# Kernel tuning notes

Hardware: AMD Instinct MI355X
Metric: run time of the kernel (lower is better)

The kernel has to match this reference:

```python
import jax, jax.numpy as jnp
import numpy as np

B, N, D_IN, D, K, H, ITERS = 128, 4096, 64, 64, 8, 128, 3
SCALE = D ** -0.5
EPS_ATTN = 1e-8
EPS_LN = 1e-5


def layer_norm(x, g, b):
    m = jnp.mean(x, axis=-1, keepdims=True)
    v = jnp.mean((x - m) ** 2, axis=-1, keepdims=True)
    return (x - m) * jax.lax.rsqrt(v + EPS_LN) * g + b


def setup_inputs() -> dict:
    key = jax.random.key(0)
    ks = jax.random.split(key, 16)
    s = 0.05
    return {
        "inputs": jax.random.normal(ks[0], (B, N, D_IN), dtype=jnp.float32),
        "noise": jax.random.normal(ks[1], (B, K, D), dtype=jnp.float32),
        "slots_mu": jax.random.normal(ks[2], (1, 1, D), dtype=jnp.float32),
        "slots_sigma": jax.random.normal(ks[3], (1, 1, D), dtype=jnp.float32),
        "Wq": jax.random.normal(ks[4], (D, D), dtype=jnp.float32) * s,
        "Wk": jax.random.normal(ks[5], (D_IN, D), dtype=jnp.float32) * s,
        "Wv": jax.random.normal(ks[6], (D_IN, D), dtype=jnp.float32) * s,
        "W_ih": jax.random.normal(ks[7], (3 * D, D), dtype=jnp.float32) * s,
        "W_hh": jax.random.normal(ks[8], (3 * D, D), dtype=jnp.float32) * s,
        "b_ih": jnp.zeros((3 * D,), dtype=jnp.float32),
        "b_hh": jnp.zeros((3 * D,), dtype=jnp.float32),
        "mlp_W1": jax.random.normal(ks[9], (D, H), dtype=jnp.float32) * s,
        "mlp_b1": jnp.zeros((H,), dtype=jnp.float32),
        "mlp_W2": jax.random.normal(ks[10], (H, D), dtype=jnp.float32) * s,
        "mlp_b2": jnp.zeros((D,), dtype=jnp.float32),
        "ln_in_g": jnp.ones((D_IN,), dtype=jnp.float32),
        "ln_in_b": jnp.zeros((D_IN,), dtype=jnp.float32),
        "ln_s_g": jnp.ones((D,), dtype=jnp.float32),
        "ln_s_b": jnp.zeros((D,), dtype=jnp.float32),
        "ln_ff_g": jnp.ones((D,), dtype=jnp.float32),
        "ln_ff_b": jnp.zeros((D,), dtype=jnp.float32),
    }


def reference(inputs, noise, slots_mu, slots_sigma, Wq, Wk, Wv,
              W_ih, W_hh, b_ih, b_hh, mlp_W1, mlp_b1, mlp_W2, mlp_b2,
              ln_in_g, ln_in_b, ln_s_g, ln_s_b, ln_ff_g, ln_ff_b):
    # slots = Normal(mu, sigma) with externally supplied standard noise
    slots = slots_mu + slots_sigma * noise                      # [B,K,D]
    x = layer_norm(inputs, ln_in_g, ln_in_b)                     # [B,N,D_IN]
    k = x @ Wk                                                   # [B,N,D]
    v = x @ Wv                                                   # [B,N,D]

    for _ in range(ITERS):
        slots_prev = slots
        s = layer_norm(slots, ln_s_g, ln_s_b)
        q = s @ Wq                                               # [B,K,D]
        dots = jnp.einsum('bid,bjd->bij', q, k) * SCALE          # [B,K,N]
        attn = jax.nn.softmax(dots, axis=1) + EPS_ATTN           # softmax over slots
        attn_n = attn / jnp.sum(attn, axis=-1, keepdims=True)
        updates = jnp.einsum('bjd,bij->bid', v, attn_n)          # [B,K,D]

        # single-step GRU (torch nn.GRU gate order: reset, update, new)
        gx = updates @ W_ih.T + b_ih                             # [B,K,3D]
        gh = slots_prev @ W_hh.T + b_hh                          # [B,K,3D]
        gx_r, gx_z, gx_n = jnp.split(gx, 3, axis=-1)
        gh_r, gh_z, gh_n = jnp.split(gh, 3, axis=-1)
        r = jax.nn.sigmoid(gx_r + gh_r)
        z = jax.nn.sigmoid(gx_z + gh_z)
        n = jnp.tanh(gx_n + r * gh_n)
        slots = (1.0 - z) * n + z * slots_prev

        slots = layer_norm(slots, ln_ff_g, ln_ff_b)
        slots = slots + (jax.nn.relu(slots @ mlp_W1 + mlp_b1) @ mlp_W2 + mlp_b2)
    return slots
```

## Files before the change

kernel.cpp:

```cpp
#include <hip/hip_runtime.h>
#include <hip/hip_bf16.h>

typedef unsigned int u32;
typedef unsigned short u16;
typedef __attribute__((ext_vector_type(8))) short short8;
typedef __attribute__((ext_vector_type(4))) float f32x4;
typedef __attribute__((ext_vector_type(2))) u32 u32x2;

#define B_      128
#define N_      4096
#define K_      8
#define SCALE_  0.125f
#define EPS_A   1e-8f
#define EPS_LN  1e-5f

__device__ __forceinline__ float bf_lo(u32 u){ union{u32 v; float f;} x; x.v = u<<16; return x.f; }
__device__ __forceinline__ u16 f2bf(float f){
  union{float f; u32 v;} x; x.f = f;
  u32 v = x.v;
  return (u16)((v + 0x7fffu + ((v>>16)&1u))>>16);
}
__device__ __forceinline__ float wsum64(float v){
  #pragma unroll
  for (int off=32; off; off>>=1) v += __shfl_xor(v, off, 64);
  return v;
}
__device__ __forceinline__ void gll16(const void* g, void* l){
  __builtin_amdgcn_global_load_lds(
      (const __attribute__((address_space(1))) void*)g,
      (__attribute__((address_space(3))) void*)l, 16, 0, 0);
}

__global__ void prep_t(const float* __restrict__ Wih, const float* __restrict__ Whh,
                       const float* __restrict__ Wq,  const float* __restrict__ Wk,
                       float* __restrict__ WihT, float* __restrict__ WhhT,
                       float* __restrict__ Wqk, int* __restrict__ flags){
  int t = threadIdx.x;
  if (blockIdx.x == 0 && t < B_) flags[t] = 0;
  if (blockIdx.x < 48){
    int idx = blockIdx.x*256 + t;
    int g = idx>>6, d = idx&63;
    WihT[d*192+g] = Wih[idx];
    WhhT[d*192+g] = Whh[idx];
  } else {
    __shared__ float WkL[64*65];
    int bi = blockIdx.x - 48;
    #pragma unroll
    for (int k=0;k<16;++k){
      int idx = t + k*256;
      int d = idx>>6, m = idx&63;
      WkL[m*65+d] = Wk[idx];
    }
    __syncthreads();
    int a = bi*4 + (t>>6), d = t&63;
    float acc = 0.f;
    #pragma unroll 8
    for (int m=0;m<64;++m) acc += Wq[a*64+m]*WkL[m*65+d];
    Wqk[a*64+d] = acc;
  }
}

__device__ __forceinline__ void tile_attn(
    char* ibuf, char* abuf, short8 qf0, short8 qf1,
    int fr, int fq, f32x4* c2, float* tsl)
{
  f32x4 c1[2];
  __builtin_amdgcn_s_setprio(1);
  #pragma unroll
  for (int nt=0;nt<2;++nt){
    c1[nt] = (f32x4){0.f,0.f,0.f,0.f};
    #pragma unroll
    for (int kk=0;kk<2;++kk){
      int byte = ((kk*2+(fq>>1))<<10) | (((fr>>2)&1)<<9)
               | ((nt*2+(fr>>3))<<7) | ((fr&3)<<5) | ((fq&1)<<4);
      short8 xf = *(const short8*)(ibuf + byte);
      c1[nt] = __builtin_amdgcn_mfma_f32_16x16x32_bf16(kk?qf1:qf0, xf, c1[nt], 0,0,0);
    }
  }
  __builtin_amdgcn_s_setprio(0);
  #pragma unroll
  for (int nt=0;nt<2;++nt){
    float d0 = c1[nt][0]*SCALE_, d1 = c1[nt][1]*SCALE_;
    float d2 = c1[nt][2]*SCALE_, d3 = c1[nt][3]*SCALE_;
    float m = fmaxf(fmaxf(d0,d1), fmaxf(d2,d3));
    m = fmaxf(m, __shfl_xor(m, 16, 64));
    float e0 = __expf(d0-m), e1 = __expf(d1-m), e2 = __expf(d2-m), e3 = __expf(d3-m);
    float sl = e0+e1+e2+e3;
    float inv = 1.f/(sl + __shfl_xor(sl, 16, 64));
    float a0 = e0*inv + EPS_A, a1 = e1*inv + EPS_A;
    float a2 = e2*inv + EPS_A, a3 = e3*inv + EPS_A;
    tsl[0]+=a0; tsl[1]+=a1; tsl[2]+=a2; tsl[3]+=a3;
    int pos2 = (nt*16 + fr)*2;
    *(u16*)(abuf + (((fq*4+0)*64 + pos2) ^ (0<<4))) = f2bf(a0);
    *(u16*)(abuf + (((fq*4+1)*64 + pos2) ^ (1<<4))) = f2bf(a1);
    *(u16*)(abuf + (((fq*4+2)*64 + pos2) ^ (2<<4))) = f2bf(a2);
    *(u16*)(abuf + (((fq*4+3)*64 + pos2) ^ (3<<4))) = f2bf(a3);
  }
  asm volatile("s_waitcnt lgkmcnt(0)" ::: "memory");
  __builtin_amdgcn_sched_barrier(0);
  {
    short8 pa = *(const short8*)(abuf + ((fr*64 + fq*16) ^ ((fr&3)<<4)));
    u32 va = (u32)(size_t)ibuf + (fq<<7) + (fr<<1);
    u32x2 tv0,tv1,tv2,tv3,tv4,tv5,tv6,tv7;
    asm volatile("ds_read_b64_tr_b16 %0, %1 offset:0"    : "=v"(tv0) : "v"(va));
    asm volatile("ds_read_b64_tr_b16 %0, %1 offset:512"  : "=v"(tv1) : "v"(va));
    asm volatile("ds_read_b64_tr_b16 %0, %1 offset:1024" : "=v"(tv2) : "v"(va));
    asm volatile("ds_read_b64_tr_b16 %0, %1 offset:1536" : "=v"(tv3) : "v"(va));
    asm volatile("ds_read_b64_tr_b16 %0, %1 offset:2048" : "=v"(tv4) : "v"(va));
    asm volatile("ds_read_b64_tr_b16 %0, %1 offset:2560" : "=v"(tv5) : "v"(va));
    asm volatile("ds_read_b64_tr_b16 %0, %1 offset:3072" : "=v"(tv6) : "v"(va));
    asm volatile("ds_read_b64_tr_b16 %0, %1 offset:3584" : "=v"(tv7) : "v"(va));
    asm volatile("s_waitcnt lgkmcnt(0)" ::: "memory");
    __builtin_amdgcn_sched_barrier(0);
    union { short8 s8; u32 u4[4]; } xb;
    __builtin_amdgcn_s_setprio(1);
    xb.u4[0]=tv0.x; xb.u4[1]=tv0.y; xb.u4[2]=tv1.x; xb.u4[3]=tv1.y;
    c2[0] = __builtin_amdgcn_mfma_f32_16x16x32_bf16(pa, xb.s8, c2[0], 0,0,0);
    xb.u4[0]=tv2.x; xb.u4[1]=tv2.y; xb.u4[2]=tv3.x; xb.u4[3]=tv3.y;
    c2[1] = __builtin_amdgcn_mfma_f32_16x16x32_bf16(pa, xb.s8, c2[1], 0,0,0);
    xb.u4[0]=tv4.x; xb.u4[1]=tv4.y; xb.u4[2]=tv5.x; xb.u4[3]=tv5.y;
    c2[2] = __builtin_amdgcn_mfma_f32_16x16x32_bf16(pa, xb.s8, c2[2], 0,0,0);
    xb.u4[0]=tv6.x; xb.u4[1]=tv6.y; xb.u4[2]=tv7.x; xb.u4[3]=tv7.y;
    c2[3] = __builtin_amdgcn_mfma_f32_16x16x32_bf16(pa, xb.s8, c2[3], 0,0,0);
    __builtin_amdgcn_s_setprio(0);
  }
}

__global__ __launch_bounds__(512,1) void fused_sa(
    const float* __restrict__ inp, u16* __restrict__ xhat,
    const float* __restrict__ noise, const float* __restrict__ mu, const float* __restrict__ sigma,
    const float* __restrict__ Wqk,
    const float* __restrict__ lng, const float* __restrict__ lnb,
    const float* __restrict__ lnsg, const float* __restrict__ lnsb,
    const float* __restrict__ WihT, const float* __restrict__ WhhT,
    const float* __restrict__ bih, const float* __restrict__ bhh,
    const float* __restrict__ W1, const float* __restrict__ b1,
    const float* __restrict__ W2, const float* __restrict__ b2,
    const float* __restrict__ lnffg, const float* __restrict__ lnffb,
    const float* __restrict__ Wv,
    float* __restrict__ PUg, float* __restrict__ PSg, int* __restrict__ flags,
    float* __restrict__ dout)
{
  __shared__ __align__(16) char smem[152320];
  int bid = blockIdx.x, t = threadIdx.x;
  int b = bid & 127, half = bid >> 7;
  int w = t>>6, lane = t&63;
  int fr = lane&15, fq = lane>>4;
  int i = w, d = lane;

  char*  wbase = smem + w*9216;
  char*  abuf  = wbase + 8192;
  char*  qA    = smem + 73728;
  float* UL    = (float*)(smem + 75776);
  float* SL    = (float*)(smem + 92160);
  u16*   wih_l = (u16*)(smem + 92416);
  u16*   whh_l = (u16*)(smem + 116992);
  float* updL  = (float*)(smem + 141568);
  float* spL   = (float*)(smem + 143744);
  float* sfL   = (float*)(smem + 145920);
  float* hL    = (float*)(smem + 148096);

  {
    const float4* wa = (const float4*)WihT;
    const float4* wb = (const float4*)WhhT;
    #pragma unroll
    for (int k2=0;k2<6;++k2){
      int idx = t + k2*512;
      float4 va = wa[idx], vb = wb[idx];
      ((u32*)wih_l)[idx*2]   = (u32)f2bf(va.x) | ((u32)f2bf(va.y)<<16);
      ((u32*)wih_l)[idx*2+1] = (u32)f2bf(va.z) | ((u32)f2bf(va.w)<<16);
      ((u32*)whh_l)[idx*2]   = (u32)f2bf(vb.x) | ((u32)f2bf(vb.y)<<16);
      ((u32*)whh_l)[idx*2+1] = (u32)f2bf(vb.z) | ((u32)f2bf(vb.w)<<16);
    }
  }
  if (t < 256) ((u32*)(qA + 1024))[t] = 0;
  float sp = mu[d] + sigma[d]*noise[b*512 + t];
  {
    float m  = wsum64(sp)*(1.f/64.f);
    float df = sp - m;
    float vv = wsum64(df*df)*(1.f/64.f);
    float sv = df*rsqrtf(vv+EPS_LN)*lnsg[d] + lnsb[d];
    updL[i*68+d] = sv;
  }
  __syncthreads();
  {
    float qt = 0.f;
    #pragma unroll 8
    for (int dd=0; dd<64; ++dd) qt += updL[i*68+dd]*Wqk[dd*64 + d];
    *(u16*)(qA + ((i*128 + d*2) ^ ((i&7)<<4))) = f2bf(qt);
  }
  __syncthreads();

  long tbase = (long)b*128 + half*64 + w*8;

  for (int it=0; it<3; ++it){
    f32x4 c2[4];
    #pragma unroll
    for (int k2=0;k2<4;++k2) c2[k2] = (f32x4){0.f,0.f,0.f,0.f};
    float tsl[4] = {0.f,0.f,0.f,0.f};
    short8 qf0 = *(const short8*)(qA + ((fr*128 +  0 + fq*16) ^ ((fr&7)<<4)));
    short8 qf1 = *(const short8*)(qA + ((fr*128 + 64 + fq*16) ^ ((fr&7)<<4)));

    if (it == 0){
      for (int tile=0; tile<8; ++tile){
        char* ibuf = wbase;
        {
          int r = lane>>1, hx = lane&1;
          const float4* xr = (const float4*)(inp +
              ((long)b*N_ + half*2048 + w*256 + tile*32 + r)*64 + hx*32);
          float xv[32]; float s=0.f, sq=0.f;
          #pragma unroll
          for (int c=0;c<8;++c){
            float4 f = xr[c];
            xv[c*4+0]=f.x; xv[c*4+1]=f.y; xv[c*4+2]=f.z; xv[c*4+3]=f.w;
            s  += f.x+f.y+f.z+f.w;
            sq += f.x*f.x+f.y*f.y+f.z*f.z+f.w*f.w;
          }
          s  += __shfl_xor(s,1,64);
          sq += __shfl_xor(sq,1,64);
          float mean = s*(1.f/64.f);
          float inv  = rsqrtf(sq*(1.f/64.f) - mean*mean + EPS_LN);
          float lgv[32], lbv[32];
          {
            const float4* g4 = (const float4*)(lng + hx*32);
            const float4* b4 = (const float4*)(lnb + hx*32);
            #pragma unroll
            for (int e=0;e<8;++e){
              float4 gv = g4[e], bv = b4[e];
              lgv[e*4+0]=gv.x; lgv[e*4+1]=gv.y; lgv[e*4+2]=gv.z; lgv[e*4+3]=gv.w;
              lbv[e*4+0]=bv.x; lbv[e*4+1]=bv.y; lbv[e*4+2]=bv.z; lbv[e*4+3]=bv.w;
            }
          }
          u32 pk[16];
          #pragma unroll
          for (int e=0;e<16;++e){
            float a0 = (xv[e*2]  -mean)*inv*lgv[e*2]   + lbv[e*2];
            float a1 = (xv[e*2+1]-mean)*inv*lgv[e*2+1] + lbv[e*2+1];
            pk[e] = (u32)f2bf(a0) | ((u32)f2bf(a1)<<16);
          }
          int pbits = (((r>>2)&1)<<9) | (((r>>3)&3)<<7) | ((r&3)<<5);
          #pragma unroll
          for (int hf=0; hf<2; ++hf){
            int dt = hx*2 + hf;
            uint4 v0; v0.x=pk[hf*8+0]; v0.y=pk[hf*8+1]; v0.z=pk[hf*8+2]; v0.w=pk[hf*8+3];
            uint4 v1; v1.x=pk[hf*8+4]; v1.y=pk[hf*8+5]; v1.z=pk[hf*8+6]; v1.w=pk[hf*8+7];
            *(uint4*)(ibuf + ((dt<<10) | pbits))      = v0;
            *(uint4*)(ibuf + ((dt<<10) | pbits) + 16) = v1;
          }
          asm volatile("s_waitcnt lgkmcnt(0)" ::: "memory");
          __builtin_amdgcn_sched_barrier(0);
          char* gim = (char*)xhat + ((tbase+tile)<<12) + lane*16;
          #pragma unroll
          for (int j=0;j<4;++j)
            *(uint4*)(gim + j*1024) = *(const uint4*)(ibuf + lane*16 + j*1024);
        }
        tile_attn(ibuf, abuf, qf0, qf1, fr, fq, c2, tsl);
      }
      asm volatile("s_waitcnt vmcnt(0)" ::: "memory");
      __builtin_amdgcn_sched_barrier(0);
    } else {
      {
        const char* g0 = (const char*)xhat + (tbase<<12) + lane*16;
        #pragma unroll
        for (int j=0;j<4;++j) gll16(g0 + j*1024, wbase + j*1024);
      }
      #pragma unroll 2
      for (int tile=0; tile<8; ++tile){
        char* ibuf = wbase + (tile&1)*4096;
        if (tile < 7){
          const char* gn = (const char*)xhat + ((tbase+tile+1)<<12) + lane*16;
          char* ln = wbase + ((tile+1)&1)*4096;
          #pragma unroll
          for (int j=0;j<4;++j) gll16(gn + j*1024, ln + j*1024);
          asm volatile("s_waitcnt vmcnt(4)" ::: "memory");
        } else {
          asm volatile("s_waitcnt vmcnt(0)" ::: "memory");
        }
        __builtin_amdgcn_sched_barrier(0);
        tile_attn(ibuf, abuf, qf0, qf1, fr, fq, c2, tsl);
      }
    }
    if (fq < 2){
      #pragma unroll
      for (int dblk=0;dblk<4;++dblk){
        #pragma unroll
        for (int r2=0;r2<4;++r2)
          UL[w*512 + (fq*4+r2)*64 + dblk*16 + fr] = c2[dblk][r2];
      }
    }
    #pragma unroll
    for (int mk=1; mk<16; mk<<=1){
      tsl[0] += __shfl_xor(tsl[0], mk, 64);
      tsl[1] += __shfl_xor(tsl[1], mk, 64);
      tsl[2] += __shfl_xor(tsl[2], mk, 64);
      tsl[3] += __shfl_xor(tsl[3], mk, 64);
    }
    if (fr==0 && fq<2){
      SL[w*8 + fq*4+0] = tsl[0]; SL[w*8 + fq*4+1] = tsl[1];
      SL[w*8 + fq*4+2] = tsl[2]; SL[w*8 + fq*4+3] = tsl[3];
    }
    __syncthreads();

    float u = 0.f, S = 0.f;
    #pragma unroll
    for (int cw=0; cw<8; ++cw){
      u += UL[cw*512 + i*64 + d];
      S += SL[cw*8 + i];
    }
    {
      long pbase = ((long)it*256 + bid);
      __hip_atomic_store(&PUg[pbase*512 + t], u, __ATOMIC_RELAXED, __HIP_MEMORY_SCOPE_AGENT);
      if (d == 0)
        __hip_atomic_store(&PSg[pbase*8 + i], S, __ATOMIC_RELAXED, __HIP_MEMORY_SCOPE_AGENT);
    }
    asm volatile("s_waitcnt vmcnt(0)" ::: "memory");
    __syncthreads();
    if (t == 0){
      __hip_atomic_fetch_add(&flags[b], 1, __ATOMIC_RELAXED, __HIP_MEMORY_SCOPE_AGENT);
      while (__hip_atomic_load(&flags[b], __ATOMIC_RELAXED, __HIP_MEMORY_SCOPE_AGENT) < 2*(it+1))
        __builtin_amdgcn_s_sleep(2);
    }
    __syncthreads();
    {
      long obase = ((long)it*256 + (bid ^ 128));
      u += __hip_atomic_load(&PUg[obase*512 + t], __ATOMIC_RELAXED, __HIP_MEMORY_SCOPE_AGENT);
      S += __hip_atomic_load(&PSg[obase*8 + i], __ATOMIC_RELAXED, __HIP_MEMORY_SCOPE_AGENT);
    }

    float ut = u / S;
    sfL[i*68+d] = ut;
    spL[i*68+d] = sp;
    __syncthreads();
    float upd = 0.f;
    #pragma unroll 8
    for (int dd=0; dd<64; ++dd) upd += sfL[i*68+dd]*Wv[dd*64 + d];
    updL[i*68+d] = upd;
    __syncthreads();
    float gx0 = bih[d], gx1 = bih[64+d], gx2 = bih[128+d];
    float gh0 = bhh[d], gh1 = bhh[64+d], gh2 = bhh[128+d];
    #pragma unroll 8
    for (int dd=0; dd<64; ++dd){
      float uv = updL[i*68+dd];
      float sv = spL[i*68+dd];
      gx0 += uv*bf_lo((u32)wih_l[dd*192 + d]);
      gx1 += uv*bf_lo((u32)wih_l[dd*192 + 64 + d]);
      gx2 += uv*bf_lo((u32)wih_l[dd*192 + 128 + d]);
      gh0 += sv*bf_lo((u32)whh_l[dd*192 + d]);
      gh1 += sv*bf_lo((u32)whh_l[dd*192 + 64 + d]);
      gh2 += sv*bf_lo((u32)whh_l[dd*192 + 128 + d]);
    }
    float rg = 1.f/(1.f+__expf(-(gx0+gh0)));
    float zg = 1.f/(1.f+__expf(-(gx1+gh1)));
    float ng = tanhf(gx2 + rg*gh2);
    float sn = (1.f-zg)*ng + zg*sp;
    float m1 = wsum64(sn)*(1.f/64.f);
    float df = sn-m1;
    float vv = wsum64(df*df)*(1.f/64.f);
    float sf = df*rsqrtf(vv+EPS_LN)*lnffg[d] + lnffb[d];
    sfL[i*68+d] = sf;
    __syncthreads();
    float h0 = b1[d], h1 = b1[64+d];
    #pragma unroll 8
    for (int dd=0;dd<64;++dd){
      float sv = sfL[i*68+dd];
      h0 += sv*W1[dd*128 + d];
      h1 += sv*W1[dd*128 + 64 + d];
    }
    h0 = fmaxf(h0, 0.f); h1 = fmaxf(h1, 0.f);
    hL[i*132+d] = h0; hL[i*132+64+d] = h1;
    __syncthreads();
    float o = b2[d];
    #pragma unroll 8
    for (int hh=0; hh<128; ++hh) o += hL[i*132+hh]*W2[hh*64 + d];
    float out = sf + o;
    sp = out;
    if (it == 2){
      if (half == 0) dout[b*512 + t] = out;
    } else {
      float m2 = wsum64(out)*(1.f/64.f);
      float d2 = out-m2;
      float v2 = wsum64(d2*d2)*(1.f/64.f);
      float sq = d2*rsqrtf(v2+EPS_LN)*lnsg[d] + lnsb[d];
      updL[i*68+d] = sq;
      __syncthreads();
      float qt = 0.f;
      #pragma unroll 8
      for (int dd=0;dd<64;++dd) qt += updL[i*68+dd]*Wqk[dd*64 + d];
      *(u16*)(qA + ((i*128 + d*2) ^ ((i&7)<<4))) = f2bf(qt);
      __syncthreads();
    }
  }
}

extern "C" void kernel_launch(void* const* d_in, const int* in_sizes, int n_in,
                              void* d_out, int out_size, void* d_ws, size_t ws_size,
                              hipStream_t stream){
  const float* inp   = (const float*)d_in[0];
  const float* noise = (const float*)d_in[1];
  const float* mu    = (const float*)d_in[2];
  const float* sigma = (const float*)d_in[3];
  const float* Wq    = (const float*)d_in[4];
  const float* Wk    = (const float*)d_in[5];
  const float* Wv    = (const float*)d_in[6];
  const float* Wih   = (const float*)d_in[7];
  const float* Whh   = (const float*)d_in[8];
  const float* bih   = (const float*)d_in[9];
  const float* bhh   = (const float*)d_in[10];
  const float* W1    = (const float*)d_in[11];
  const float* b1    = (const float*)d_in[12];
  const float* W2    = (const float*)d_in[13];
  const float* b2    = (const float*)d_in[14];
  const float* lnig  = (const float*)d_in[15];
  const float* lnib  = (const float*)d_in[16];
  const float* lnsg  = (const float*)d_in[17];
  const float* lnsb  = (const float*)d_in[18];
  const float* lnffg = (const float*)d_in[19];
  const float* lnffb = (const float*)d_in[20];
  float* out = (float*)d_out;

  char* ws = (char*)d_ws;
  u16*   xhat  = (u16*)(ws);
  float* WihT  = (float*)(ws + 67108864);
  float* WhhT  = (float*)(ws + 67158016);
  float* Wqk   = (float*)(ws + 67207168);
  float* PUg   = (float*)(ws + 67223552);
  float* PSg   = (float*)(ws + 68796416);
  int*   flags = (int*)(ws + 68820992);

  prep_t<<<64,256,0,stream>>>(Wih, Whh, Wq, Wk, WihT, WhhT, Wqk, flags);
  fused_sa<<<2*B_,512,0,stream>>>(inp, xhat, noise, mu, sigma, Wqk,
                                  lnig, lnib, lnsg, lnsb,
                                  WihT, WhhT, bih, bhh,
                                  W1, b1, W2, b2, lnffg, lnffb, Wv,
                                  PUg, PSg, flags, out);
}
```

Measured before the change: 131.8 us.

## Split input layernorm into a separate wide kernel before fused slot attention

The input layernorm and bf16 packing of the 128x4096x64 input move out of the first iteration of the fused kernel into a standalone kernel launched over 4096 blocks. The fused kernel then uses the same double-buffered prefetch path in every iteration. The aim is to use the whole GPU's bandwidth for the big fp32 read, since the fused kernel only runs 256 blocks. The cost is an extra launch and a round trip of the bf16 copy through memory, where the old first iteration could overlap this work with attention.

```diff
diff --git a/kernel.cpp b/kernel.cpp
--- a/kernel.cpp
+++ b/kernel.cpp
@@ -58,6 +58,65 @@
     for (int m=0;m<64;++m) acc += Wq[a*64+m]*WkL[m*65+d];
     Wqk[a*64+d] = acc;
   }
+}
+
+__global__ __launch_bounds__(256) void ln_kernel(
+    const float* __restrict__ inp,
+    const float* __restrict__ lng, const float* __restrict__ lnb,
+    u16* __restrict__ xhat){
+  __shared__ __align__(16) char smem[16384];
+  int b = blockIdx.y, t = threadIdx.x;
+  int w = t>>6, lane = t&63;
+  int tidx = blockIdx.x*4 + w;
+  char* ibuf = smem + w*4096;
+
+  int r = lane>>1, hx = lane&1;
+  const float4* xr = (const float4*)(inp + ((long)b*N_ + tidx*32 + r)*64 + hx*32);
+  float xv[32]; float s=0.f, sq=0.f;
+  #pragma unroll
+  for (int c=0;c<8;++c){
+    float4 f = xr[c];
+    xv[c*4+0]=f.x; xv[c*4+1]=f.y; xv[c*4+2]=f.z; xv[c*4+3]=f.w;
+    s  += f.x+f.y+f.z+f.w;
+    sq += f.x*f.x+f.y*f.y+f.z*f.z+f.w*f.w;
+  }
+  s  += __shfl_xor(s,1,64);
+  sq += __shfl_xor(sq,1,64);
+  float mean = s*(1.f/64.f);
+  float inv  = rsqrtf(sq*(1.f/64.f) - mean*mean + EPS_LN);
+  float lgv[32], lbv[32];
+  {
+    const float4* g4 = (const float4*)(lng + hx*32);
+    const float4* b4 = (const float4*)(lnb + hx*32);
+    #pragma unroll
+    for (int e=0;e<8;++e){
+      float4 gv = g4[e], bv = b4[e];
+      lgv[e*4+0]=gv.x; lgv[e*4+1]=gv.y; lgv[e*4+2]=gv.z; lgv[e*4+3]=gv.w;
+      lbv[e*4+0]=bv.x; lbv[e*4+1]=bv.y; lbv[e*4+2]=bv.z; lbv[e*4+3]=bv.w;
+    }
+  }
+  u32 pk[16];
+  #pragma unroll
+  for (int e=0;e<16;++e){
+    float a0 = (xv[e*2]  -mean)*inv*lgv[e*2]   + lbv[e*2];
+    float a1 = (xv[e*2+1]-mean)*inv*lgv[e*2+1] + lbv[e*2+1];
+    pk[e] = (u32)f2bf(a0) | ((u32)f2bf(a1)<<16);
+  }
+  int pbits = (((r>>2)&1)<<9) | (((r>>3)&3)<<7) | ((r&3)<<5);
+  #pragma unroll
+  for (int hf=0; hf<2; ++hf){
+    int dt = hx*2 + hf;
+    uint4 v0; v0.x=pk[hf*8+0]; v0.y=pk[hf*8+1]; v0.z=pk[hf*8+2]; v0.w=pk[hf*8+3];
+    uint4 v1; v1.x=pk[hf*8+4]; v1.y=pk[hf*8+5]; v1.z=pk[hf*8+6]; v1.w=pk[hf*8+7];
+    *(uint4*)(ibuf + ((dt<<10) | pbits))      = v0;
+    *(uint4*)(ibuf + ((dt<<10) | pbits) + 16) = v1;
+  }
+  asm volatile("s_waitcnt lgkmcnt(0)" ::: "memory");
+  __builtin_amdgcn_sched_barrier(0);
+  char* gim = (char*)xhat + (((long)b*128 + tidx)<<12) + lane*16;
+  #pragma unroll
+  for (int j=0;j<4;++j)
+    *(uint4*)(gim + j*1024) = *(const uint4*)(ibuf + lane*16 + j*1024);
 }
 
 __device__ __forceinline__ void tile_attn(
@@ -127,10 +186,9 @@
 }
 
 __global__ __launch_bounds__(512,1) void fused_sa(
-    const float* __restrict__ inp, u16* __restrict__ xhat,
+    u16* __restrict__ xhat,
     const float* __restrict__ noise, const float* __restrict__ mu, const float* __restrict__ sigma,
     const float* __restrict__ Wqk,
-    const float* __restrict__ lng, const float* __restrict__ lnb,
     const float* __restrict__ lnsg, const float* __restrict__ lnsb,
     const float* __restrict__ WihT, const float* __restrict__ WhhT,
     const float* __restrict__ bih, const float* __restrict__ bhh,
@@ -201,84 +259,25 @@
     short8 qf0 = *(const short8*)(qA + ((fr*128 +  0 + fq*16) ^ ((fr&7)<<4)));
     short8 qf1 = *(const short8*)(qA + ((fr*128 + 64 + fq*16) ^ ((fr&7)<<4)));
 
-    if (it == 0){
-      for (int tile=0; tile<8; ++tile){
-        char* ibuf = wbase;
-        {
-          int r = lane>>1, hx = lane&1;
-          const float4* xr = (const float4*)(inp +
-              ((long)b*N_ + half*2048 + w*256 + tile*32 + r)*64 + hx*32);
-          float xv[32]; float s=0.f, sq=0.f;
-          #pragma unroll
-          for (int c=0;c<8;++c){
-            float4 f = xr[c];
-            xv[c*4+0]=f.x; xv[c*4+1]=f.y; xv[c*4+2]=f.z; xv[c*4+3]=f.w;
-            s  += f.x+f.y+f.z+f.w;
-            sq += f.x*f.x+f.y*f.y+f.z*f.z+f.w*f.w;
-          }
-          s  += __shfl_xor(s,1,64);
-          sq += __shfl_xor(sq,1,64);
-          float mean = s*(1.f/64.f);
-          float inv  = rsqrtf(sq*(1.f/64.f) - mean*mean + EPS_LN);
-          float lgv[32], lbv[32];
-          {
-            const float4* g4 = (const float4*)(lng + hx*32);
-            const float4* b4 = (const float4*)(lnb + hx*32);
-            #pragma unroll
-            for (int e=0;e<8;++e){
-              float4 gv = g4[e], bv = b4[e];
-              lgv[e*4+0]=gv.x; lgv[e*4+1]=gv.y; lgv[e*4+2]=gv.z; lgv[e*4+3]=gv.w;
-              lbv[e*4+0]=bv.x; lbv[e*4+1]=bv.y; lbv[e*4+2]=bv.z; lbv[e*4+3]=bv.w;
-            }
-          }
-          u32 pk[16];
-          #pragma unroll
-          for (int e=0;e<16;++e){
-            float a0 = (xv[e*2]  -mean)*inv*lgv[e*2]   + lbv[e*2];
-            float a1 = (xv[e*2+1]-mean)*inv*lgv[e*2+1] + lbv[e*2+1];
-            pk[e] = (u32)f2bf(a0) | ((u32)f2bf(a1)<<16);
-          }
-          int pbits = (((r>>2)&1)<<9) | (((r>>3)&3)<<7) | ((r&3)<<5);
-          #pragma unroll
-          for (int hf=0; hf<2; ++hf){
-            int dt = hx*2 + hf;
-            uint4 v0; v0.x=pk[hf*8+0]; v0.y=pk[hf*8+1]; v0.z=pk[hf*8+2]; v0.w=pk[hf*8+3];
-            uint4 v1; v1.x=pk[hf*8+4]; v1.y=pk[hf*8+5]; v1.z=pk[hf*8+6]; v1.w=pk[hf*8+7];
-            *(uint4*)(ibuf + ((dt<<10) | pbits))      = v0;
-            *(uint4*)(ibuf + ((dt<<10) | pbits) + 16) = v1;
-          }
-          asm volatile("s_waitcnt lgkmcnt(0)" ::: "memory");
-          __builtin_amdgcn_sched_barrier(0);
-          char* gim = (char*)xhat + ((tbase+tile)<<12) + lane*16;
-          #pragma unroll
-          for (int j=0;j<4;++j)
-            *(uint4*)(gim + j*1024) = *(const uint4*)(ibuf + lane*16 + j*1024);
-        }
-        tile_attn(ibuf, abuf, qf0, qf1, fr, fq, c2, tsl);
+    {
+      const char* g0 = (const char*)xhat + (tbase<<12) + lane*16;
+      #pragma unroll
+      for (int j=0;j<4;++j) gll16(g0 + j*1024, wbase + j*1024);
+    }
+    #pragma unroll 2
+    for (int tile=0; tile<8; ++tile){
+      char* ibuf = wbase + (tile&1)*4096;
+      if (tile < 7){
+        const char* gn = (const char*)xhat + ((tbase+tile+1)<<12) + lane*16;
+        char* ln = wbase + ((tile+1)&1)*4096;
+        #pragma unroll
+        for (int j=0;j<4;++j) gll16(gn + j*1024, ln + j*1024);
+        asm volatile("s_waitcnt vmcnt(4)" ::: "memory");
+      } else {
+        asm volatile("s_waitcnt vmcnt(0)" ::: "memory");
       }
-      asm volatile("s_waitcnt vmcnt(0)" ::: "memory");
       __builtin_amdgcn_sched_barrier(0);
-    } else {
-      {
-        const char* g0 = (const char*)xhat + (tbase<<12) + lane*16;
-        #pragma unroll
-        for (int j=0;j<4;++j) gll16(g0 + j*1024, wbase + j*1024);
-      }
-      #pragma unroll 2
-      for (int tile=0; tile<8; ++tile){
-        char* ibuf = wbase + (tile&1)*4096;
-        if (tile < 7){
-          const char* gn = (const char*)xhat + ((tbase+tile+1)<<12) + lane*16;
-          char* ln = wbase + ((tile+1)&1)*4096;
-          #pragma unroll
-          for (int j=0;j<4;++j) gll16(gn + j*1024, ln + j*1024);
-          asm volatile("s_waitcnt vmcnt(4)" ::: "memory");
-        } else {
-          asm volatile("s_waitcnt vmcnt(0)" ::: "memory");
-        }
-        __builtin_amdgcn_sched_barrier(0);
-        tile_attn(ibuf, abuf, qf0, qf1, fr, fq, c2, tsl);
-      }
+      tile_attn(ibuf, abuf, qf0, qf1, fr, fq, c2, tsl);
     }
     if (fq < 2){
       #pragma unroll
@@ -428,8 +427,9 @@
   int*   flags = (int*)(ws + 68820992);
 
   prep_t<<<64,256,0,stream>>>(Wih, Whh, Wq, Wk, WihT, WhhT, Wqk, flags);
-  fused_sa<<<2*B_,512,0,stream>>>(inp, xhat, noise, mu, sigma, Wqk,
-                                  lnig, lnib, lnsg, lnsb,
+  ln_kernel<<<dim3(32,B_),256,0,stream>>>(inp, lnig, lnib, xhat);
+  fused_sa<<<2*B_,512,0,stream>>>(xhat, noise, mu, sigma, Wqk,
+                                  lnsg, lnsb,
                                   WihT, WhhT, bih, bhh,
                                   W1, b1, W2, b2, lnffg, lnffb, Wv,
                                   PUg, PSg, flags, out);
```

Result: slower. 142.3 us (+7.9%).
